# Optimization experiments

Measured on AMD Instinct MI355X. Metric: run time of the kernel, lower is better.

Reference implementation:

```python
import jax, jax.numpy as jnp
import numpy as np

T, B, N_IN, H, N_OUT = 32, 32, 64, 256, 64
CLAMP_MIN, CLAMP_MAX = -2.0, 2.0  # scalar `min`/`max` forward args of the torch module


def setup_inputs() -> dict:
    key = jax.random.key(0)
    ks = jax.random.split(key, 8)
    s_ih = 1.0 / np.sqrt(N_IN)
    s_hh = 1.0 / np.sqrt(H)
    X = jax.random.normal(ks[0], (T, B, N_IN), jnp.float32)
    eps = jax.random.uniform(ks[1], (B,), jnp.float32) * 0.1  # per-sample perturbation radius
    W_ih = jax.random.normal(ks[2], (N_IN, H), jnp.float32) * s_ih  # already transposed, as in forward
    W_hh = jax.random.normal(ks[3], (H, H), jnp.float32) * s_hh
    b_ih = jax.random.normal(ks[4], (H,), jnp.float32) * s_hh
    b_hh = jax.random.normal(ks[5], (H,), jnp.float32) * s_hh
    W_o = jax.random.normal(ks[6], (H, N_OUT), jnp.float32) * s_hh
    b_o = jax.random.normal(ks[7], (N_OUT,), jnp.float32) * s_hh
    return dict(X=X, eps=eps, W_ih=W_ih, W_hh=W_hh, b_ih=b_ih, b_hh=b_hh, W_o=W_o, b_o=b_o)


def _zono_tanh(head, err):
    # DeepZ-style abstract tanh transformer on a zonotope (head [B,H], err [B,E,H]).
    rad = jnp.sum(jnp.abs(err), axis=1)                  # [B,H] concretization radius
    l, u = head - rad, head + rad
    tl, tu = jnp.tanh(l), jnp.tanh(u)
    lam = jnp.minimum(1.0 - tl * tl, 1.0 - tu * tu)      # minimal slope on [l,u]
    mu = 0.5 * (tu + tl - lam * (u + l))
    delta = 0.5 * (tu - tl - lam * (u - l))              # new error magnitude (>=0)
    new_head = lam * head + mu
    new_err = jnp.concatenate([lam[:, None, :] * err,
                               jax.vmap(jnp.diag)(delta)], axis=1)  # append H fresh symbols
    return new_head, new_err


def reference(X, eps, W_ih, W_hh, b_ih, b_hh, W_o, b_o):
    Bsz, Hn = X.shape[1], W_hh.shape[0]
    head_h = jnp.zeros((Bsz, Hn), X.dtype)
    err_h = jnp.zeros((Bsz, 0, Hn), X.dtype)
    bias = b_ih + b_hh
    for t in range(X.shape[0]):  # sequential recurrence; T is static
        x = X[t]                                          # [B, N_IN]
        l = jnp.maximum(x - eps[:, None], CLAMP_MIN)      # clamp(x-eps, min=min)
        u = jnp.minimum(x + eps[:, None], CLAMP_MAX)      # clamp(x+eps, max=max)
        head_x = 0.5 * (l + u)
        err_x = jax.vmap(jnp.diag)(0.5 * (u - l))         # diag_embed -> [B, N_IN, N_IN]
        # affine zonotope step: hx + hi + b_ih + b_hh
        head = head_x @ W_ih + head_h @ W_hh + bias       # [B, H]
        err = jnp.concatenate([err_h @ W_hh, err_x @ W_ih], axis=1)  # [B, E+N_IN, H]
        head_h, err_h = _zono_tanh(head, err)
    # output layer on the final zonotope; return concretized [lower, upper] bounds
    head_out = head_h @ W_o + b_o                         # [B, N_OUT]
    rad_out = jnp.sum(jnp.abs(err_h @ W_o), axis=1)       # [B, N_OUT]
    return jnp.stack([head_out - rad_out, head_out + rad_out])  # [2, B, N_OUT]
```

## Files before the change

### kernel.cpp

```cpp
#include <hip/hip_runtime.h>
#include <math.h>

typedef unsigned short u16;
typedef unsigned long long u64;
typedef __attribute__((ext_vector_type(8))) short bf16x8;
typedef __attribute__((ext_vector_type(4))) float f32x4;

#define T_STEPS 32
#define BSZ     32
#define N_IN    64
#define H       256
#define N_OUT   64
#define ESTRIDE 9984
#define CLAMP_MIN (-2.0f)
#define CLAMP_MAX ( 2.0f)
#define GNB 16


__device__ inline u16 f2bf(float x) {
    unsigned u = __builtin_bit_cast(unsigned, x);
    unsigned r = u + 0x7FFFu + ((u >> 16) & 1u);
    return (u16)(r >> 16);
}
__device__ inline float bf2f(short s) {
    return __builtin_bit_cast(float, ((unsigned)(u16)s) << 16);
}

__device__ __forceinline__ void gl_lds16(const u16* g, u16* l) {
    __builtin_amdgcn_global_load_lds(
        (const __attribute__((address_space(1))) unsigned int*)g,
        (__attribute__((address_space(3))) unsigned int*)l,
        16, 0, 0);
}

__device__ __forceinline__ float aload(const float* p) {
    return __hip_atomic_load(p, __ATOMIC_RELAXED, __HIP_MEMORY_SCOPE_AGENT);
}

__global__ void initarr_k(unsigned* arr) {
    arr[threadIdx.x + blockIdx.x * 256] = 0u;
}

__global__ void transpose_k(const float* __restrict__ src, float* __restrict__ dst,
                            int R, int C)
{
    __shared__ float tile[32][33];
    int bi = blockIdx.y, bj = blockIdx.x;
    int r0 = threadIdx.x >> 5, c = threadIdx.x & 31;
    #pragma unroll
    for (int rr = 0; rr < 4; ++rr) {
        int r = r0 * 4 + rr;
        tile[r][c] = src[(bi * 32 + r) * C + bj * 32 + c];
    }
    __syncthreads();
    #pragma unroll
    for (int rr = 0; rr < 4; ++rr) {
        int r = r0 * 4 + rr;
        dst[(bj * 32 + r) * R + bi * 32 + c] = tile[c][r];
    }
}

__global__ void packPairs_k(const float* __restrict__ W, float* __restrict__ WP)
{
    int p = blockIdx.x * 256 + threadIdx.x;
    int vb = (p & 1) * 2, hh = (p >> 1) & 1, m = (p >> 2) & 15, qq = (p >> 6) & 3;
    int KC = (p >> 8) & 7, RT = p >> 11;
    int i = RT * 16 + m, k = KC * 32 + qq * 8 + hh * 4 + vb;
    ((float2*)WP)[p] = make_float2(W[(size_t)i * H + k], W[(size_t)i * H + k + 1]);
}

__global__ void packWT_k(const float* __restrict__ WT32, u16* __restrict__ WTp)
{
    int p = blockIdx.x * 256 + threadIdx.x;
    int vb = (p & 1) * 2, hh = (p >> 1) & 1, m = (p >> 2) & 15, qq = (p >> 6) & 3;
    int KC = (p >> 8) & 7, RT = p >> 11;
    int n = RT * 16 + m, k = KC * 32 + qq * 8 + hh * 4 + vb;
    *(unsigned*)&WTp[2 * p] =
          (unsigned)f2bf(WT32[(size_t)n * H + k])
        | ((unsigned)f2bf(WT32[(size_t)n * H + k + 1]) << 16);
}

__global__ __launch_bounds__(256) void prefresh_k(
    const float* __restrict__ X, const float* __restrict__ eps,
    const float* __restrict__ Wih, const float* __restrict__ WihP,
    const float* __restrict__ bih, const float* __restrict__ bhh,
    u16* __restrict__ err, float* __restrict__ radT, float* __restrict__ hpX)
{
    __shared__ float rho_s[N_IN], hx_s[N_IN];
    const int t = blockIdx.x, bi = blockIdx.y, tid = threadIdx.x;
    if (tid < N_IN) {
        float x = X[((size_t)t * BSZ + bi) * N_IN + tid], e = eps[bi];
        float lo = fmaxf(x - e, CLAMP_MIN), up = fminf(x + e, CLAMP_MAX);
        rho_s[tid] = 0.5f * (up - lo);
        hx_s[tid]  = 0.5f * (up + lo);
    }
    __syncthreads();

    float s = 0.f, acc = bih[tid] + bhh[tid];
    #pragma unroll 8
    for (int i = 0; i < N_IN; ++i) {
        float w = Wih[(size_t)i * H + tid];
        s   += fabsf(rho_s[i]) * fabsf(w);
        acc += hx_s[i] * w;
    }
    radT[(size_t)t * BSZ * H + (size_t)bi * H + tid] = s;
    hpX [(size_t)t * BSZ * H + (size_t)bi * H + tid] = acc;

    u16* dst = err + (size_t)bi * ESTRIDE * H + (size_t)(20 * t) * 4096;
    const float2* wp = (const float2*)WihP;
    #pragma unroll 4
    for (int iter = 0; iter < 32; ++iter) {
        int p = iter * 256 + tid;
        int i = (p >> 11) * 16 + ((p >> 2) & 15);
        float2 w = wp[p];
        float rho = rho_s[i];
        *(unsigned*)&dst[2 * p] =
            (unsigned)f2bf(rho * w.x) | ((unsigned)f2bf(rho * w.y) << 16);
    }
}

__global__ __launch_bounds__(256, 2) void loop_k(
    const float* __restrict__ Whh, const float* __restrict__ WhhP,
    const u16* __restrict__ WhhTp,
    float* __restrict__ hpX, float* __restrict__ radT,
    u16* __restrict__ err, unsigned* __restrict__ arrive, int b0)
{
    __shared__ u16 sbuf[4][8192];
    __shared__ float lam_s[H], de_s[H], hh_s[H];
    const int bx = blockIdx.x, b = blockIdx.y, tid = threadIdx.x;
    const int babs = b0 + b;
    u16* errB = err + (size_t)b * ESTRIDE * H;
    const int wave = tid >> 6, lane = tid & 63;
    const int m = lane & 15, q = lane >> 4;

    #pragma unroll 1
    for (int t = 1; t < T_STEPS; ++t) {
        const int E_old = t * (N_IN + H);
        const int ntiles = (E_old - H) >> 5;
        const float* hpp  = hpX  + (size_t)(t - 1) * BSZ * H + (size_t)babs * H;
        float*       hpn  = hpX  + (size_t)t       * BSZ * H + (size_t)babs * H;
        const float* radp = radT + (size_t)(t - 1) * BSZ * H + (size_t)babs * H;
        float*       radn = radT + (size_t)t       * BSZ * H + (size_t)babs * H;
        const bool gem = (bx < ntiles);

        if (gem) {
            #pragma unroll
            for (int j = 0; j < 3; ++j) {
                int tj = bx + j * GNB;
                if (tj < ntiles) {
                    const u16* g = errB + (size_t)tj * 8192;
                    #pragma unroll
                    for (int r = 0; r < 4; ++r)
                        gl_lds16(g + r * 2048 + tid * 8,
                                 &sbuf[j][r * 2048 + wave * 512]);
                }
            }
        }
        bf16x8 bf[4][8];
        if (gem) {
            #pragma unroll
            for (int nt = 0; nt < 4; ++nt)
                #pragma unroll
                for (int kc = 0; kc < 8; ++kc)
                    bf[nt][kc] = *(const bf16x8*)
                        &WhhTp[(size_t)(((((wave * 4 + nt) * 8 + kc) * 4 + q) << 7) + m * 8)];
        }

        if (t > 1) {
            if (tid == 0) {
                const unsigned* a = &arrive[(t - 1) * BSZ + babs];
                while (__hip_atomic_load(a, __ATOMIC_RELAXED,
                                         __HIP_MEMORY_SCOPE_AGENT) < (unsigned)GNB)
                    __builtin_amdgcn_s_sleep(16);
            }
            __builtin_amdgcn_s_barrier();
        }

        {
            float hd = aload(&hpp[tid]), rv = aload(&radp[tid]);
            float lo = hd - rv, up = hd + rv;
            float tl = tanhf(lo), tu = tanhf(up);
            float la = fminf(1.f - tl * tl, 1.f - tu * tu);
            float mu = 0.5f * (tu + tl - la * (up + lo));
            float dd = 0.5f * (tu - tl - la * (up - lo));
            lam_s[tid] = la;
            de_s[tid]  = dd;
            hh_s[tid]  = la * hd + mu;
        }
        asm volatile("s_waitcnt lgkmcnt(0)" ::: "memory");
        __builtin_amdgcn_s_barrier();

        if (gem) {
            #pragma unroll
            for (int nt = 0; nt < 4; ++nt)
                #pragma unroll
                for (int kc = 0; kc < 8; ++kc) {
                    const int k0 = kc * 32 + q * 8;
                    float4 la = *(const float4*)&lam_s[k0];
                    float4 lb = *(const float4*)&lam_s[k0 + 4];
                    bf16x8 w = bf[nt][kc], f;
                    f[0] = (short)f2bf(bf2f(w[0]) * la.x);
                    f[1] = (short)f2bf(bf2f(w[1]) * la.y);
                    f[2] = (short)f2bf(bf2f(w[2]) * la.z);
                    f[3] = (short)f2bf(bf2f(w[3]) * la.w);
                    f[4] = (short)f2bf(bf2f(w[4]) * lb.x);
                    f[5] = (short)f2bf(bf2f(w[5]) * lb.y);
                    f[6] = (short)f2bf(bf2f(w[6]) * lb.z);
                    f[7] = (short)f2bf(bf2f(w[7]) * lb.w);
                    bf[nt][kc] = f;
                }

            float racc[16];
            #pragma unroll
            for (int i = 0; i < 16; ++i) racc[i] = 0.f;

            asm volatile("s_waitcnt vmcnt(0)" ::: "memory");
            __builtin_amdgcn_s_barrier();

            int cur = 0;
            for (int tile = bx; tile < ntiles; tile += GNB) {
                int pf = tile + 3 * GNB;
                if (pf < ntiles) {
                    const u16* g = errB + (size_t)pf * 8192;
                    #pragma unroll
                    for (int r = 0; r < 4; ++r)
                        gl_lds16(g + r * 2048 + tid * 8,
                                 &sbuf[(cur + 3) & 3][r * 2048 + wave * 512]);
                }

                f32x4 acc[2][4];
                #pragma unroll
                for (int i = 0; i < 2; ++i)
                    #pragma unroll
                    for (int c = 0; c < 4; ++c) acc[i][c] = (f32x4){0.f, 0.f, 0.f, 0.f};

                #pragma unroll
                for (int kc = 0; kc < 8; ++kc) {
                    bf16x8 af[2];
                    #pragma unroll
                    for (int rt = 0; rt < 2; ++rt)
                        af[rt] = *(const bf16x8*)
                            &sbuf[cur][(((rt * 8 + kc) * 4 + q) << 7) + m * 8];
                    #pragma unroll
                    for (int nt = 0; nt < 4; ++nt)
                        #pragma unroll
                        for (int rt = 0; rt < 2; ++rt)
                            acc[rt][nt] = __builtin_amdgcn_mfma_f32_16x16x32_bf16(
                                bf[nt][kc], af[rt], acc[rt][nt], 0, 0, 0);
                }

                #pragma unroll
                for (int rt = 0; rt < 2; ++rt) {
                    const size_t rowbase = (size_t)(tile * 2 + rt) * 4096;
                    #pragma unroll
                    for (int nt = 0; nt < 4; ++nt) {
                        f32x4 v = acc[rt][nt];
                        racc[nt * 4 + 0] += fabsf(v[0]);
                        racc[nt * 4 + 1] += fabsf(v[1]);
                        racc[nt * 4 + 2] += fabsf(v[2]);
                        racc[nt * 4 + 3] += fabsf(v[3]);
                        unsigned lo = (unsigned)f2bf(v[0]) | ((unsigned)f2bf(v[1]) << 16);
                        unsigned hi = (unsigned)f2bf(v[2]) | ((unsigned)f2bf(v[3]) << 16);
                        const int NT  = wave * 4 + nt;
                        const int kcs = NT >> 1;
                        const int qq  = (NT & 1) * 2 + (q >> 1);
                        const size_t off16 = rowbase
                            + (size_t)(((kcs * 4 + qq) << 7) + m * 8 + (q & 1) * 4);
                        *(u64*)&errB[off16] = ((u64)hi << 32) | lo;
                    }
                }
                asm volatile("s_waitcnt vmcnt(32)" ::: "memory");
                __builtin_amdgcn_s_barrier();
                cur = (cur + 1) & 3;
            }

            #pragma unroll
            for (int i = 0; i < 16; ++i) {
                float v = racc[i];
                v += __shfl_xor(v, 1);
                v += __shfl_xor(v, 2);
                v += __shfl_xor(v, 4);
                v += __shfl_xor(v, 8);
                if (m == 0) {
                    int nt = i >> 2, vv = i & 3;
                    atomicAdd(&radn[wave * 64 + nt * 16 + q * 4 + vv], v);
                }
            }
        }

        const int dtile0 = 10 * t - 8;
        const float2* wp = (const float2*)WhhP;
        #pragma unroll
        for (int i = 0; i < 8; ++i) {
            int dt = dtile0 + i;
            if ((dt & 15) == bx) {
                #pragma unroll
                for (int rt2 = 0; rt2 < 2; ++rt2) {
                    int RTw = i * 2 + rt2;
                    u16* dst2 = errB + (size_t)(dt * 2 + rt2) * 4096;
                    const float2* wp2 = wp + (size_t)RTw * 2048;
                    #pragma unroll
                    for (int iter = 0; iter < 8; ++iter) {
                        int p = iter * 256 + tid;
                        int mm = (p >> 2) & 15;
                        float dv = de_s[RTw * 16 + mm];
                        float2 w = wp2[p];
                        *(unsigned*)&dst2[2 * p] =
                            (unsigned)f2bf(dv * w.x) | ((unsigned)f2bf(dv * w.y) << 16);
                    }
                }
            }
        }
        float s = 0.f, hacc = 0.f;
        #pragma unroll
        for (int ii = 0; ii < 16; ++ii) {
            int i = bx * 16 + ii;
            float w = Whh[(size_t)i * H + tid];
            s    += fabsf(de_s[i]) * fabsf(w);
            hacc += hh_s[i] * w;
        }
        atomicAdd(&radn[tid], s);
        atomicAdd(&hpn[tid], hacc);

        asm volatile("s_waitcnt vmcnt(0)" ::: "memory");
        __syncthreads();
        if (tid == 0)
            __hip_atomic_fetch_add(&arrive[t * BSZ + babs], 1u,
                                   __ATOMIC_RELAXED, __HIP_MEMORY_SCOPE_AGENT);
    }
}

__global__ __launch_bounds__(256) void tanh_final_k(
    const float* __restrict__ hp, const float* __restrict__ rad,
    float* __restrict__ lam, float* __restrict__ de, float* __restrict__ head_h)
{
    const int b = blockIdx.x, h = threadIdx.x;
    float hd = hp[b * H + h], r = rad[b * H + h];
    float l = hd - r, u = hd + r;
    float tl = tanhf(l), tu = tanhf(u);
    float la = fminf(1.f - tl * tl, 1.f - tu * tu);
    float mu = 0.5f * (tu + tl - la * (u + l));
    float dd = 0.5f * (tu - tl - la * (u - l));
    lam[b * H + h] = la;
    de[b * H + h]  = dd;
    head_h[b * H + h] = la * hd + mu;
}

__global__ __launch_bounds__(256) void packWoT_k(
    const float* __restrict__ WoT32, const float* __restrict__ lam,
    u16* __restrict__ WoTp)
{
    const int b = blockIdx.x, tid = threadIdx.x;
    __shared__ float lam_s[H];
    lam_s[tid] = lam[b * H + tid];
    __syncthreads();
    u16* dst = WoTp + (size_t)b * N_OUT * H;
    #pragma unroll 4
    for (int iter = 0; iter < 32; ++iter) {
        int p = iter * 256 + tid;
        int vb = (p & 1) * 2, hh = (p >> 1) & 1, m = (p >> 2) & 15, qq = (p >> 6) & 3;
        int KC = (p >> 8) & 7, RT = p >> 11;
        int n = RT * 16 + m, k = KC * 32 + qq * 8 + hh * 4 + vb;
        *(unsigned*)&dst[2 * p] =
              (unsigned)f2bf(lam_s[k]     * WoT32[(size_t)n * H + k])
            | ((unsigned)f2bf(lam_s[k + 1] * WoT32[(size_t)n * H + k + 1]) << 16);
    }
}

__global__ void head_out_k(
    const float* __restrict__ head_h, const float* __restrict__ de,
    const float* __restrict__ Wo, const float* __restrict__ bo,
    float* __restrict__ head_out, float* __restrict__ rad_out)
{
    const int b = blockIdx.x, o = threadIdx.x;
    float acc = bo[o], accR = 0.f;
    #pragma unroll 4
    for (int j = 0; j < H; ++j) {
        float w = Wo[j * N_OUT + o];
        acc  += head_h[b * H + j] * w;
        accR += fabsf(de[b * H + j] * w);
    }
    head_out[b * N_OUT + o] = acc;
    rad_out[b * N_OUT + o]  = accR;
}

__global__ __launch_bounds__(256) void gemm_out_k(
    const u16* __restrict__ err, const u16* __restrict__ WoTp,
    float* __restrict__ rad_out)
{
    __shared__ float rad_s[N_OUT];
    const int b = blockIdx.y, row0 = blockIdx.x * 256, tid = threadIdx.x;
    const int wave = tid >> 6, lane = tid & 63;
    const int m = lane & 15, q = lane >> 4;
    const u16* errB = err + (size_t)b * ESTRIDE * H;
    const u16* Wb   = WoTp + (size_t)b * N_OUT * H;

    if (tid < N_OUT) rad_s[tid] = 0.f;
    __syncthreads();

    f32x4 acc[4][4];
    #pragma unroll
    for (int i = 0; i < 4; ++i)
        #pragma unroll
        for (int c = 0; c < 4; ++c) acc[i][c] = (f32x4){0.f, 0.f, 0.f, 0.f};

    const int tile0 = (row0 >> 4) + wave * 4;
    #pragma unroll
    for (int kc = 0; kc < 8; ++kc) {
        bf16x8 af[4], bw[4];
        #pragma unroll
        for (int rt = 0; rt < 4; ++rt)
            af[rt] = *(const bf16x8*)
                &errB[(size_t)(((((tile0 + rt) * 8 + kc) * 4 + q) << 7) + m * 8)];
        #pragma unroll
        for (int nt = 0; nt < 4; ++nt)
            bw[nt] = *(const bf16x8*)
                &Wb[(size_t)((((nt * 8 + kc) * 4 + q) << 7) + m * 8)];
        #pragma unroll
        for (int nt = 0; nt < 4; ++nt)
            #pragma unroll
            for (int rt = 0; rt < 4; ++rt)
                acc[rt][nt] = __builtin_amdgcn_mfma_f32_16x16x32_bf16(
                    af[rt], bw[nt], acc[rt][nt], 0, 0, 0);
    }
    #pragma unroll
    for (int nt = 0; nt < 4; ++nt) {
        float s = 0.f;
        #pragma unroll
        for (int rt = 0; rt < 4; ++rt)
            #pragma unroll
            for (int r = 0; r < 4; ++r) s += fabsf(acc[rt][nt][r]);
        atomicAdd(&rad_s[nt * 16 + m], s);
    }
    __syncthreads();
    if (tid < N_OUT) atomicAdd(&rad_out[b * N_OUT + tid], rad_s[tid]);
}

__global__ void combine_k(const float* __restrict__ head_out,
                          const float* __restrict__ rad_out,
                          float* __restrict__ out)
{
    int i = blockIdx.x * 256 + threadIdx.x;
    if (i < BSZ * N_OUT) {
        float h = head_out[i], r = rad_out[i];
        out[i]               = h - r;
        out[BSZ * N_OUT + i] = h + r;
    }
}

extern "C" void kernel_launch(void* const* d_in, const int* in_sizes, int n_in,
                              void* d_out, int out_size, void* d_ws, size_t ws_size,
                              hipStream_t stream)
{
    const float* X    = (const float*)d_in[0];
    const float* eps  = (const float*)d_in[1];
    const float* Wih  = (const float*)d_in[2];
    const float* Whh  = (const float*)d_in[3];
    const float* bih  = (const float*)d_in[4];
    const float* bhh  = (const float*)d_in[5];
    const float* Wo   = (const float*)d_in[6];
    const float* bo   = (const float*)d_in[7];
    float* out = (float*)d_out;

    const size_t per_sample = (size_t)ESTRIDE * H * 2 + (size_t)N_OUT * H * 2;
    const size_t shared_b = (size_t)H * H * 4
                          + (size_t)N_OUT * H * 4
                          + (size_t)N_IN * H * 4
                          + (size_t)H * H * 4
                          + (size_t)H * H * 2
                          + (size_t)T_STEPS * BSZ * H * 4
                          + (size_t)T_STEPS * BSZ * H * 4
                          + (size_t)3 * BSZ * H * 4
                          + (size_t)2 * BSZ * N_OUT * 4
                          + (size_t)T_STEPS * BSZ * 4 + 512;
    int Bc = BSZ;
    while (Bc > 1 && (size_t)Bc * per_sample + shared_b > ws_size) Bc >>= 1;

    char* p = (char*)d_ws;
    u16* errP      = (u16*)p;   p += (size_t)Bc * ESTRIDE * H * 2;
    u16* WoTp      = (u16*)p;   p += (size_t)Bc * N_OUT * H * 2;
    u16* WhhTp     = (u16*)p;   p += (size_t)H * H * 2;
    float* WhhT32  = (float*)p; p += (size_t)H * H * 4;
    float* WoT32   = (float*)p; p += (size_t)N_OUT * H * 4;
    float* WihP    = (float*)p; p += (size_t)N_IN * H * 4;
    float* WhhP    = (float*)p; p += (size_t)H * H * 4;
    float* hpX     = (float*)p; p += (size_t)T_STEPS * BSZ * H * 4;
    float* radT    = (float*)p; p += (size_t)T_STEPS * BSZ * H * 4;
    float* lam     = (float*)p; p += (size_t)BSZ * H * 4;
    float* de      = (float*)p; p += (size_t)BSZ * H * 4;
    float* head_h  = (float*)p; p += (size_t)BSZ * H * 4;
    float* head_out= (float*)p; p += (size_t)BSZ * N_OUT * 4;
    float* rad_out = (float*)p; p += (size_t)BSZ * N_OUT * 4 + 64;
    unsigned* arrive = (unsigned*)p;

    initarr_k<<<(T_STEPS * BSZ) / 256, 256, 0, stream>>>(arrive);
    transpose_k<<<dim3(H / 32, H / 32), 256, 0, stream>>>(Whh, WhhT32, H, H);
    transpose_k<<<dim3(N_OUT / 32, H / 32), 256, 0, stream>>>(Wo, WoT32, H, N_OUT);
    packPairs_k<<<(N_IN * 128) / 256, 256, 0, stream>>>(Wih, WihP);
    packPairs_k<<<(H * 128) / 256, 256, 0, stream>>>(Whh, WhhP);
    packWT_k<<<128, 256, 0, stream>>>(WhhT32, WhhTp);

    for (int b0 = 0; b0 < BSZ; b0 += Bc) {
        prefresh_k<<<dim3(T_STEPS, Bc), 256, 0, stream>>>(
            X + (size_t)b0 * N_IN, eps + b0, Wih, WihP, bih, bhh, errP,
            radT + (size_t)b0 * H, hpX + (size_t)b0 * H);

        loop_k<<<dim3(GNB, Bc), 256, 0, stream>>>(
            Whh, WhhP, WhhTp, hpX, radT, errP, arrive, b0);

        const float* hp_last  = hpX  + (size_t)(T_STEPS - 1) * BSZ * H + (size_t)b0 * H;
        const float* rad_last = radT + (size_t)(T_STEPS - 1) * BSZ * H + (size_t)b0 * H;
        tanh_final_k<<<Bc, 256, 0, stream>>>(
            hp_last, rad_last, lam + (size_t)b0 * H, de + (size_t)b0 * H,
            head_h + (size_t)b0 * H);
        packWoT_k<<<Bc, 256, 0, stream>>>(WoT32, lam + (size_t)b0 * H, WoTp);
        head_out_k<<<Bc, 64, 0, stream>>>(
            head_h + (size_t)b0 * H, de + (size_t)b0 * H, Wo, bo,
            head_out + (size_t)b0 * N_OUT, rad_out + (size_t)b0 * N_OUT);
        gemm_out_k<<<dim3(ESTRIDE / 256, Bc), 256, 0, stream>>>(
            errP, WoTp, rad_out + (size_t)b0 * N_OUT);
    }

    combine_k<<<(BSZ * N_OUT + 255) / 256, 256, 0, stream>>>(head_out, rad_out, out);
}
```

Measured before the change: 1.702 ms.

## Interleave two batch samples per workgroup and widen tile split to 32 slices

Each workgroup in the recurrent loop kernel now alternates between two batch samples (pb and pb+Bc2), with 32 column-slices per sample instead of 16 and half as many workgroup rows. The next half-step's error tiles are prefetched into LDS before the current step's fresh-symbol writes and partial head/radius sums, so one sample's wait on its cross-workgroup arrival counter can overlap with the other sample's work. This is meant to hide the per-timestep global spin-barrier latency and spread the GEMM over more workgroups. The cost is more complex control flow, more atomics per step, and a dependence on NSL being a power of two for the diagonal-tile ownership mask.

After: 2.352 ms. 1.38x slower.

```diff
diff --git a/kernel.cpp b/kernel.cpp
--- a/kernel.cpp
+++ b/kernel.cpp
@@ -14,7 +14,7 @@
 #define ESTRIDE 9984
 #define CLAMP_MIN (-2.0f)
 #define CLAMP_MAX ( 2.0f)
-#define GNB 16
+#define NSL 32
 
 
 __device__ inline u16 f2bf(float x) {
@@ -35,6 +35,23 @@
 
 __device__ __forceinline__ float aload(const float* p) {
     return __hip_atomic_load(p, __ATOMIC_RELAXED, __HIP_MEMORY_SCOPE_AGENT);
+}
+
+__device__ __forceinline__ void stage3(const u16* errS, u16 (*sbuf)[8192],
+                                       int ntiles, int bx, int cur,
+                                       int tid, int wave)
+{
+    #pragma unroll
+    for (int j = 0; j < 3; ++j) {
+        int tj = bx + j * NSL;
+        if (tj < ntiles) {
+            const u16* g = errS + (size_t)tj * 8192;
+            #pragma unroll
+            for (int r = 0; r < 4; ++r)
+                gl_lds16(g + r * 2048 + tid * 8,
+                         &sbuf[(cur + j) & 3][r * 2048 + wave * 512]);
+        }
+    }
 }
 
 __global__ void initarr_k(unsigned* arr) {
@@ -123,39 +140,37 @@
     const float* __restrict__ Whh, const float* __restrict__ WhhP,
     const u16* __restrict__ WhhTp,
     float* __restrict__ hpX, float* __restrict__ radT,
-    u16* __restrict__ err, unsigned* __restrict__ arrive, int b0)
+    u16* __restrict__ err, unsigned* __restrict__ arrive,
+    int b0, int Bc, int Bc2)
 {
     __shared__ u16 sbuf[4][8192];
     __shared__ float lam_s[H], de_s[H], hh_s[H];
-    const int bx = blockIdx.x, b = blockIdx.y, tid = threadIdx.x;
-    const int babs = b0 + b;
-    u16* errB = err + (size_t)b * ESTRIDE * H;
+    const int bx = blockIdx.x, pb = blockIdx.y, tid = threadIdx.x;
     const int wave = tid >> 6, lane = tid & 63;
     const int m = lane & 15, q = lane >> 4;
 
+    int cur = 0;
+    {
+        const u16* errS = err + (size_t)pb * ESTRIDE * H;
+        stage3(errS, sbuf, 2, bx, cur, tid, wave);
+    }
+
     #pragma unroll 1
-    for (int t = 1; t < T_STEPS; ++t) {
+    for (int h = 0; h < 2 * (T_STEPS - 1); ++h) {
+        const int t  = (h >> 1) + 1;
+        const int s  = h & 1;
+        const int bb = s ? pb + Bc2 : pb;
+        const bool act = (bb < Bc);
+        const int babs = b0 + bb;
+        u16* errS = err + (size_t)bb * ESTRIDE * H;
         const int E_old = t * (N_IN + H);
         const int ntiles = (E_old - H) >> 5;
         const float* hpp  = hpX  + (size_t)(t - 1) * BSZ * H + (size_t)babs * H;
         float*       hpn  = hpX  + (size_t)t       * BSZ * H + (size_t)babs * H;
         const float* radp = radT + (size_t)(t - 1) * BSZ * H + (size_t)babs * H;
         float*       radn = radT + (size_t)t       * BSZ * H + (size_t)babs * H;
-        const bool gem = (bx < ntiles);
-
-        if (gem) {
-            #pragma unroll
-            for (int j = 0; j < 3; ++j) {
-                int tj = bx + j * GNB;
-                if (tj < ntiles) {
-                    const u16* g = errB + (size_t)tj * 8192;
-                    #pragma unroll
-                    for (int r = 0; r < 4; ++r)
-                        gl_lds16(g + r * 2048 + tid * 8,
-                                 &sbuf[j][r * 2048 + wave * 512]);
-                }
-            }
-        }
+        const bool gem = act && (bx < ntiles);
+
         bf16x8 bf[4][8];
         if (gem) {
             #pragma unroll
@@ -166,17 +181,17 @@
                         &WhhTp[(size_t)(((((wave * 4 + nt) * 8 + kc) * 4 + q) << 7) + m * 8)];
         }
 
-        if (t > 1) {
+        if (act && t > 1) {
             if (tid == 0) {
                 const unsigned* a = &arrive[(t - 1) * BSZ + babs];
                 while (__hip_atomic_load(a, __ATOMIC_RELAXED,
-                                         __HIP_MEMORY_SCOPE_AGENT) < (unsigned)GNB)
-                    __builtin_amdgcn_s_sleep(16);
+                                         __HIP_MEMORY_SCOPE_AGENT) < (unsigned)NSL)
+                    __builtin_amdgcn_s_sleep(8);
             }
             __builtin_amdgcn_s_barrier();
         }
 
-        {
+        if (act) {
             float hd = aload(&hpp[tid]), rv = aload(&radp[tid]);
             float lo = hd - rv, up = hd + rv;
             float tl = tanhf(lo), tu = tanhf(up);
@@ -186,9 +201,9 @@
             lam_s[tid] = la;
             de_s[tid]  = dd;
             hh_s[tid]  = la * hd + mu;
-        }
-        asm volatile("s_waitcnt lgkmcnt(0)" ::: "memory");
-        __builtin_amdgcn_s_barrier();
+            asm volatile("s_waitcnt lgkmcnt(0)" ::: "memory");
+            __builtin_amdgcn_s_barrier();
+        }
 
         if (gem) {
             #pragma unroll
@@ -217,11 +232,10 @@
             asm volatile("s_waitcnt vmcnt(0)" ::: "memory");
             __builtin_amdgcn_s_barrier();
 
-            int cur = 0;
-            for (int tile = bx; tile < ntiles; tile += GNB) {
-                int pf = tile + 3 * GNB;
+            for (int tile = bx; tile < ntiles; tile += NSL) {
+                int pf = tile + 3 * NSL;
                 if (pf < ntiles) {
-                    const u16* g = errB + (size_t)pf * 8192;
+                    const u16* g = errS + (size_t)pf * 8192;
                     #pragma unroll
                     for (int r = 0; r < 4; ++r)
                         gl_lds16(g + r * 2048 + tid * 8,
@@ -266,7 +280,7 @@
                         const int qq  = (NT & 1) * 2 + (q >> 1);
                         const size_t off16 = rowbase
                             + (size_t)(((kcs * 4 + qq) << 7) + m * 8 + (q & 1) * 4);
-                        *(u64*)&errB[off16] = ((u64)hi << 32) | lo;
+                        *(u64*)&errS[off16] = ((u64)hi << 32) | lo;
                     }
                 }
                 asm volatile("s_waitcnt vmcnt(32)" ::: "memory");
@@ -288,43 +302,58 @@
             }
         }
 
-        const int dtile0 = 10 * t - 8;
-        const float2* wp = (const float2*)WhhP;
-        #pragma unroll
-        for (int i = 0; i < 8; ++i) {
-            int dt = dtile0 + i;
-            if ((dt & 15) == bx) {
-                #pragma unroll
-                for (int rt2 = 0; rt2 < 2; ++rt2) {
-                    int RTw = i * 2 + rt2;
-                    u16* dst2 = errB + (size_t)(dt * 2 + rt2) * 4096;
-                    const float2* wp2 = wp + (size_t)RTw * 2048;
+        {
+            int hn = h + 1;
+            if (hn < 2 * (T_STEPS - 1)) {
+                int tn = (hn >> 1) + 1, sn = hn & 1;
+                int bbn = sn ? pb + Bc2 : pb;
+                if (bbn < Bc) {
+                    int ntn = (tn * (N_IN + H) - H) >> 5;
+                    stage3(err + (size_t)bbn * ESTRIDE * H, sbuf, ntn,
+                           bx, cur, tid, wave);
+                }
+            }
+        }
+
+        if (act) {
+            const int dtile0 = 10 * t - 8;
+            const float2* wp = (const float2*)WhhP;
+            #pragma unroll
+            for (int i = 0; i < 8; ++i) {
+                int dt = dtile0 + i;
+                if ((dt & (NSL - 1)) == bx) {
                     #pragma unroll
-                    for (int iter = 0; iter < 8; ++iter) {
-                        int p = iter * 256 + tid;
-                        int mm = (p >> 2) & 15;
-                        float dv = de_s[RTw * 16 + mm];
-                        float2 w = wp2[p];
-                        *(unsigned*)&dst2[2 * p] =
-                            (unsigned)f2bf(dv * w.x) | ((unsigned)f2bf(dv * w.y) << 16);
+                    for (int rt2 = 0; rt2 < 2; ++rt2) {
+                        int RTw = i * 2 + rt2;
+                        u16* dst2 = errS + (size_t)(dt * 2 + rt2) * 4096;
+                        const float2* wp2 = wp + (size_t)RTw * 2048;
+                        #pragma unroll
+                        for (int iter = 0; iter < 8; ++iter) {
+                            int p = iter * 256 + tid;
+                            int mm = (p >> 2) & 15;
+                            float dv = de_s[RTw * 16 + mm];
+                            float2 w = wp2[p];
+                            *(unsigned*)&dst2[2 * p] =
+                                (unsigned)f2bf(dv * w.x) | ((unsigned)f2bf(dv * w.y) << 16);
+                        }
                     }
                 }
             }
-        }
-        float s = 0.f, hacc = 0.f;
-        #pragma unroll
-        for (int ii = 0; ii < 16; ++ii) {
-            int i = bx * 16 + ii;
-            float w = Whh[(size_t)i * H + tid];
-            s    += fabsf(de_s[i]) * fabsf(w);
-            hacc += hh_s[i] * w;
-        }
-        atomicAdd(&radn[tid], s);
-        atomicAdd(&hpn[tid], hacc);
+            float ss = 0.f, hacc = 0.f;
+            #pragma unroll
+            for (int ii = 0; ii < 8; ++ii) {
+                int i = bx * 8 + ii;
+                float w = Whh[(size_t)i * H + tid];
+                ss   += fabsf(de_s[i]) * fabsf(w);
+                hacc += hh_s[i] * w;
+            }
+            atomicAdd(&radn[tid], ss);
+            atomicAdd(&hpn[tid], hacc);
+        }
 
         asm volatile("s_waitcnt vmcnt(0)" ::: "memory");
         __syncthreads();
-        if (tid == 0)
+        if (act && tid == 0)
             __hip_atomic_fetch_add(&arrive[t * BSZ + babs], 1u,
                                    __ATOMIC_RELAXED, __HIP_MEMORY_SCOPE_AGENT);
     }
@@ -505,8 +534,9 @@
             X + (size_t)b0 * N_IN, eps + b0, Wih, WihP, bih, bhh, errP,
             radT + (size_t)b0 * H, hpX + (size_t)b0 * H);
 
-        loop_k<<<dim3(GNB, Bc), 256, 0, stream>>>(
-            Whh, WhhP, WhhTp, hpX, radT, errP, arrive, b0);
+        int Bc2 = (Bc + 1) / 2;
+        loop_k<<<dim3(NSL, Bc2), 256, 0, stream>>>(
+            Whh, WhhP, WhhTp, hpX, radT, errP, arrive, b0, Bc, Bc2);
 
         const float* hp_last  = hpX  + (size_t)(T_STEPS - 1) * BSZ * H + (size_t)b0 * H;
         const float* rad_last = radT + (size_t)(T_STEPS - 1) * BSZ * H + (size_t)b0 * H;
```
